# Performance work log

Measured on AMD Instinct MI355X. Metric: run time of the kernel, lower is better.

Reference implementation:

```python
import jax, jax.numpy as jnp
import numpy as np

N_NODES = 100000
N_EDGES = 200000
Z_DIM = 64
ATTR_DIM = 768
HID = 128
N_CLASSES = 5


def setup_inputs() -> dict:
    key = jax.random.key(0)
    ks = jax.random.split(key, 6)
    z = jax.random.normal(ks[0], (N_NODES, Z_DIM), dtype=jnp.float32)
    edge_index = jax.random.randint(ks[1], (2, N_EDGES), 0, N_NODES, dtype=jnp.int64)
    edge_attr = jax.random.normal(ks[2], (N_EDGES, ATTR_DIM), dtype=jnp.float32)
    W1 = jax.random.normal(ks[3], (ATTR_DIM + Z_DIM, HID), dtype=jnp.float32) * 0.02
    b1 = jnp.zeros((HID,), dtype=jnp.float32)
    W2 = jax.random.normal(ks[4], (HID, N_CLASSES), dtype=jnp.float32) * 0.02
    b2 = jnp.zeros((N_CLASSES,), dtype=jnp.float32)
    return {"z": z, "edge_index": edge_index, "edge_attr": edge_attr,
            "W1": W1, "b1": b1, "W2": W2, "b2": b2}


def reference(z, edge_index, edge_attr, W1, b1, W2, b2):
    # decode(): gather endpoint embeddings, elementwise product  [E, 64]
    node_rep = z[edge_index[0]] * z[edge_index[1]]
    # concat with edge attributes -> [E, 64 + 768] (torch cat order: node_rep first)
    joint = jnp.concatenate([node_rep, edge_attr], axis=-1)
    # 2-layer MLP + softmax
    h = jax.nn.relu(joint @ W1 + b1)
    logits = h @ W2 + b2
    return jax.nn.softmax(logits, axis=-1)
```

## Files before the change

### kernel.cpp

```cpp
#include <hip/hip_runtime.h>
#include <hip/hip_bf16.h>

#define E_TOT 200000
#define NZ 64
#define ATTR_D 768
#define HID_D 128
#define NCLS 5
#define NSTG 12

typedef __attribute__((ext_vector_type(8))) short short8;
typedef __attribute__((ext_vector_type(4))) float f32x4;

typedef __attribute__((address_space(3))) unsigned       lds_u32_t;
typedef const __attribute__((address_space(1))) unsigned glob_u32_t;

__device__ __forceinline__ unsigned pk2(float a, float b) {
    __hip_bfloat162 h = __float22bfloat162_rn(make_float2(a, b));
    return *reinterpret_cast<unsigned*>(&h);
}

__device__ __forceinline__ short8 pack8(const float4 x0, const float4 x1) {
    union { unsigned u[4]; short8 s; } r;
    r.u[0] = pk2(x0.x, x0.y);
    r.u[1] = pk2(x0.z, x0.w);
    r.u[2] = pk2(x1.x, x1.y);
    r.u[3] = pk2(x1.z, x1.w);
    return r.s;
}

__global__ void prep_w1f(const float* __restrict__ W1, __hip_bfloat16* __restrict__ w1f) {
    int idx = blockIdx.x * 256 + threadIdx.x;
    if (idx >= 26 * 8 * 64 * 8) return;
    int j    = idx & 7;
    int lane = (idx >> 3) & 63;
    int f    = (idx >> 9) & 7;
    int kt   = idx >> 12;
    int n = f * 16 + (lane & 15);
    int k = kt * 32 + (lane >> 4) * 8 + j;
    w1f[idx] = __float2bfloat16(W1[(size_t)k * HID_D + n]);
}

__global__ __launch_bounds__(256, 2) void gcn_main(
    const float* __restrict__ z, const int* __restrict__ ei,
    const float* __restrict__ attr, const __hip_bfloat16* __restrict__ w1f,
    const float* __restrict__ b1, const float* __restrict__ W2,
    const float* __restrict__ b2, float* __restrict__ out) {

    __shared__ float As[2][128 * 64];

    const int t    = threadIdx.x;
    const int wv   = t >> 6;
    const int lane = t & 63;
    const int g    = lane >> 4;
    const int c0   = lane & 15;
    const int e0   = blockIdx.x * 128;

    const float* sbase[8];
#pragma unroll
    for (int i = 0; i < 8; ++i) {
        int O   = wv * 1024 + i * 4096 + lane * 16;
        int row = O >> 8;
        int c   = (O >> 4) & 15;
        int er  = e0 + row; if (er >= E_TOT) er = E_TOT - 1;
        sbase[i] = attr + (size_t)er * ATTR_D + c * 4;
    }
    auto STAGE = [&](int buf, int s) {
#pragma unroll
        for (int i = 0; i < 8; ++i)
            __builtin_amdgcn_global_load_lds(
                (glob_u32_t*)(sbase[i] + s * 64),
                (lds_u32_t*)&As[buf][wv * 256 + i * 1024],
                16, 0, 0);
    };

    const __hip_bfloat16* wf = w1f + (size_t)lane * 8;
    auto LOADB = [&](int kt, short8(&b)[8]) {
#pragma unroll
        for (int f = 0; f < 8; ++f)
            b[f] = *reinterpret_cast<const short8*>(wf + (size_t)(kt * 8 + f) * 512);
    };

    f32x4 acc[2][8];
#pragma unroll
    for (int m = 0; m < 2; ++m)
#pragma unroll
        for (int f = 0; f < 8; ++f) acc[m][f] = (f32x4){0.f, 0.f, 0.f, 0.f};

    const float* zsp[2];
    const float* zdp[2];
#pragma unroll
    for (int m = 0; m < 2; ++m) {
        int e = e0 + wv * 32 + m * 16 + c0; if (e >= E_TOT) e = E_TOT - 1;
        zsp[m] = z + (size_t)ei[e] * NZ + g * 8;
        zdp[m] = z + (size_t)ei[E_TOT + e] * NZ + g * 8;
    }
    float4 zsr[2][2][2], zdr[2][2][2];
#pragma unroll
    for (int m = 0; m < 2; ++m)
#pragma unroll
        for (int kt = 0; kt < 2; ++kt)
#pragma unroll
            for (int h = 0; h < 2; ++h) {
                zsr[m][kt][h] = *reinterpret_cast<const float4*>(zsp[m] + kt * 32 + h * 4);
                zdr[m][kt][h] = *reinterpret_cast<const float4*>(zdp[m] + kt * 32 + h * 4);
            }
    short8 bz0[8], bz1[8];
    LOADB(0, bz0); LOADB(1, bz1);
    STAGE(0, 0);

#pragma unroll
    for (int kt = 0; kt < 2; ++kt) {
        short8 a[2];
#pragma unroll
        for (int m = 0; m < 2; ++m) {
            float4 x0, x1;
            x0.x = zsr[m][kt][0].x * zdr[m][kt][0].x;
            x0.y = zsr[m][kt][0].y * zdr[m][kt][0].y;
            x0.z = zsr[m][kt][0].z * zdr[m][kt][0].z;
            x0.w = zsr[m][kt][0].w * zdr[m][kt][0].w;
            x1.x = zsr[m][kt][1].x * zdr[m][kt][1].x;
            x1.y = zsr[m][kt][1].y * zdr[m][kt][1].y;
            x1.z = zsr[m][kt][1].z * zdr[m][kt][1].z;
            x1.w = zsr[m][kt][1].w * zdr[m][kt][1].w;
            a[m] = pack8(x0, x1);
        }
#pragma unroll
        for (int f = 0; f < 8; ++f) {
            short8 bb = kt ? bz1[f] : bz0[f];
            acc[0][f] = __builtin_amdgcn_mfma_f32_16x16x32_bf16(a[0], bb, acc[0][f], 0, 0, 0);
            acc[1][f] = __builtin_amdgcn_mfma_f32_16x16x32_bf16(a[1], bb, acc[1][f], 0, 0, 0);
        }
    }

    short8 bx0[8], bx1[8], by0[8], by1[8];
    LOADB(2, bx0); LOADB(3, bx1);
    STAGE(1, 1);

#define ITER(S, BC0, BC1, BN0, BN1)                                            \
    {                                                                          \
        asm volatile("s_waitcnt vmcnt(8)" ::: "memory");                       \
        __builtin_amdgcn_sched_barrier(0);                                     \
        __builtin_amdgcn_s_barrier();                                          \
        float4 x[2][2][2];                                                     \
        _Pragma("unroll")                                                      \
        for (int m = 0; m < 2; ++m) {                                          \
            int r = wv * 32 + m * 16 + c0;                                     \
            _Pragma("unroll")                                                  \
            for (int kk = 0; kk < 2; ++kk) {                                   \
                const float* p = &As[(S) & 1][r * 64 + kk * 32 + g * 8];       \
                x[m][kk][0] = *reinterpret_cast<const float4*>(p);             \
                x[m][kk][1] = *reinterpret_cast<const float4*>(p + 4);         \
            }                                                                  \
        }                                                                      \
        asm volatile("s_waitcnt lgkmcnt(0)" ::: "memory");                     \
        __builtin_amdgcn_sched_barrier(0);                                     \
        __builtin_amdgcn_s_barrier();                                          \
        if ((S) + 1 < NSTG) { LOADB(2 * (S) + 4, BN0); LOADB(2 * (S) + 5, BN1); } \
        if ((S) + 2 < NSTG) STAGE((S) & 1, (S) + 2);                           \
        __builtin_amdgcn_sched_barrier(0);                                     \
        _Pragma("unroll")                                                      \
        for (int kk = 0; kk < 2; ++kk) {                                       \
            short8 a0 = pack8(x[0][kk][0], x[0][kk][1]);                       \
            short8 a1 = pack8(x[1][kk][0], x[1][kk][1]);                       \
            _Pragma("unroll")                                                  \
            for (int f = 0; f < 8; ++f) {                                      \
                short8 bb = kk ? (BC1)[f] : (BC0)[f];                          \
                acc[0][f] = __builtin_amdgcn_mfma_f32_16x16x32_bf16(a0, bb, acc[0][f], 0, 0, 0); \
                acc[1][f] = __builtin_amdgcn_mfma_f32_16x16x32_bf16(a1, bb, acc[1][f], 0, 0, 0); \
            }                                                                  \
        }                                                                      \
    }

    ITER(0,  bx0, bx1, by0, by1)
    ITER(1,  by0, by1, bx0, bx1)
    ITER(2,  bx0, bx1, by0, by1)
    ITER(3,  by0, by1, bx0, bx1)
    ITER(4,  bx0, bx1, by0, by1)
    ITER(5,  by0, by1, bx0, bx1)
    ITER(6,  bx0, bx1, by0, by1)
    ITER(7,  by0, by1, bx0, bx1)
    ITER(8,  bx0, bx1, by0, by1)
    ITER(9,  by0, by1, bx0, bx1)
    ITER(10, bx0, bx1, by0, by1)
    ITER(11, by0, by1, bx0, bx1)
#undef ITER

    float b1v[8], w2v[8][NCLS];
#pragma unroll
    for (int f = 0; f < 8; ++f) {
        int col = f * 16 + c0;
        b1v[f] = b1[col];
#pragma unroll
        for (int cc = 0; cc < NCLS; ++cc) w2v[f][cc] = W2[col * NCLS + cc];
    }
    float b2v[NCLS];
#pragma unroll
    for (int cc = 0; cc < NCLS; ++cc) b2v[cc] = b2[cc];

#pragma unroll
    for (int m = 0; m < 2; ++m) {
#pragma unroll
        for (int i = 0; i < 4; ++i) {
            float lg[NCLS] = {0.f, 0.f, 0.f, 0.f, 0.f};
#pragma unroll
            for (int f = 0; f < 8; ++f) {
                float h = acc[m][f][i] + b1v[f];
                h = fmaxf(h, 0.f);
#pragma unroll
                for (int cc = 0; cc < NCLS; ++cc) lg[cc] = fmaf(h, w2v[f][cc], lg[cc]);
            }
#pragma unroll
            for (int mask = 1; mask < 16; mask <<= 1) {
#pragma unroll
                for (int cc = 0; cc < NCLS; ++cc) lg[cc] += __shfl_xor(lg[cc], mask);
            }
#pragma unroll
            for (int cc = 0; cc < NCLS; ++cc) lg[cc] += b2v[cc];

            float mx = fmaxf(fmaxf(fmaxf(lg[0], lg[1]), fmaxf(lg[2], lg[3])), lg[4]);
            float q[NCLS];
            float s = 0.f;
#pragma unroll
            for (int cc = 0; cc < NCLS; ++cc) { q[cc] = __expf(lg[cc] - mx); s += q[cc]; }
            float inv = 1.0f / s;
            float num = (c0 == 0) ? q[0] : (c0 == 1) ? q[1] : (c0 == 2) ? q[2]
                      : (c0 == 3) ? q[3] : q[4];
            int eo = e0 + wv * 32 + m * 16 + g * 4 + i;
            if (eo < E_TOT && c0 < NCLS) out[(size_t)eo * NCLS + c0] = num * inv;
        }
    }
}

extern "C" void kernel_launch(void* const* d_in, const int* in_sizes, int n_in,
                              void* d_out, int out_size, void* d_ws, size_t ws_size,
                              hipStream_t stream) {
    const float* z    = (const float*)d_in[0];
    const int*   ei   = (const int*)d_in[1];
    const float* attr = (const float*)d_in[2];
    const float* W1   = (const float*)d_in[3];
    const float* b1   = (const float*)d_in[4];
    const float* W2   = (const float*)d_in[5];
    const float* b2   = (const float*)d_in[6];
    float* out = (float*)d_out;
    __hip_bfloat16* w1f = (__hip_bfloat16*)d_ws;

    prep_w1f<<<(26 * 8 * 64 * 8 + 255) / 256, 256, 0, stream>>>(W1, w1f);
    const int nblk = (E_TOT + 127) / 128;
    gcn_main<<<nblk, 256, 0, stream>>>(z, ei, attr, w1f, b1, W2, b2, out);
}
```

Baseline: 195.9 us.

## Use per-wave 4-deep swizzled LDS pipeline without block barriers

Restructures the edge_attr staging so each wave loads only its own 32 rows into a private LDS slice, which removes the block-wide s_barrier calls. The pipeline moves from a double buffer of 64-column stages to a 4-deep ring of 32-column stages with vmcnt-based waits. An XOR swizzle on the column chunks is added to avoid LDS bank conflicts, and B-fragment loads become single-buffered per stage. This is meant to cut synchronisation stalls and keep more loads in flight, in exchange for more fine-grained iterations and tighter reliance on vmcnt ordering being correct.

```diff
diff --git a/kernel.cpp b/kernel.cpp
--- a/kernel.cpp
+++ b/kernel.cpp
@@ -6,7 +6,6 @@
 #define ATTR_D 768
 #define HID_D 128
 #define NCLS 5
-#define NSTG 12
 
 typedef __attribute__((ext_vector_type(8))) short short8;
 typedef __attribute__((ext_vector_type(4))) float f32x4;
@@ -46,7 +45,7 @@
     const float* __restrict__ b1, const float* __restrict__ W2,
     const float* __restrict__ b2, float* __restrict__ out) {
 
-    __shared__ float As[2][128 * 64];
+    __shared__ float As[4][4096];
 
     const int t    = threadIdx.x;
     const int wv   = t >> 6;
@@ -55,23 +54,26 @@
     const int c0   = lane & 15;
     const int e0   = blockIdx.x * 128;
 
-    const float* sbase[8];
-#pragma unroll
-    for (int i = 0; i < 8; ++i) {
-        int O   = wv * 1024 + i * 4096 + lane * 16;
-        int row = O >> 8;
-        int c   = (O >> 4) & 15;
-        int er  = e0 + row; if (er >= E_TOT) er = E_TOT - 1;
-        sbase[i] = attr + (size_t)er * ATTR_D + c * 4;
-    }
-    auto STAGE = [&](int buf, int s) {
-#pragma unroll
-        for (int i = 0; i < 8; ++i)
-            __builtin_amdgcn_global_load_lds(
-                (glob_u32_t*)(sbase[i] + s * 64),
-                (lds_u32_t*)&As[buf][wv * 256 + i * 1024],
-                16, 0, 0);
-    };
+    const float* sbase[4];
+#pragma unroll
+    for (int i = 0; i < 4; ++i) {
+        int rsl = i * 8 + (lane >> 3);
+        int cch = (lane & 7) ^ (rsl & 7);
+        int er  = e0 + wv * 32 + rsl; if (er >= E_TOT) er = E_TOT - 1;
+        sbase[i] = attr + (size_t)er * ATTR_D + cch * 4;
+    }
+
+#define SB __builtin_amdgcn_sched_barrier(0)
+#define WAITVM(N) asm volatile("s_waitcnt vmcnt(" #N ")" ::: "memory")
+#define STAGE(BUF, S)                                                          \
+    {                                                                          \
+        _Pragma("unroll")                                                      \
+        for (int i = 0; i < 4; ++i)                                            \
+            __builtin_amdgcn_global_load_lds(                                  \
+                (glob_u32_t*)(sbase[i] + (S) * 32),                            \
+                (lds_u32_t*)&As[BUF][wv * 1024 + i * 256],                     \
+                16, 0, 0);                                                     \
+    }
 
     const __hip_bfloat16* wf = w1f + (size_t)lane * 8;
     auto LOADB = [&](int kt, short8(&b)[8]) {
@@ -79,12 +81,6 @@
         for (int f = 0; f < 8; ++f)
             b[f] = *reinterpret_cast<const short8*>(wf + (size_t)(kt * 8 + f) * 512);
     };
-
-    f32x4 acc[2][8];
-#pragma unroll
-    for (int m = 0; m < 2; ++m)
-#pragma unroll
-        for (int f = 0; f < 8; ++f) acc[m][f] = (f32x4){0.f, 0.f, 0.f, 0.f};
 
     const float* zsp[2];
     const float* zdp[2];
@@ -104,9 +100,24 @@
                 zsr[m][kt][h] = *reinterpret_cast<const float4*>(zsp[m] + kt * 32 + h * 4);
                 zdr[m][kt][h] = *reinterpret_cast<const float4*>(zdp[m] + kt * 32 + h * 4);
             }
+    SB;
     short8 bz0[8], bz1[8];
     LOADB(0, bz0); LOADB(1, bz1);
-    STAGE(0, 0);
+    SB;
+    STAGE(0, 0); SB;
+    STAGE(1, 1); SB;
+    short8 bX[8], bY[8];
+    LOADB(2, bX);
+    SB;
+    STAGE(2, 2); SB;
+    LOADB(3, bY);
+    SB;
+
+    f32x4 acc[2][8];
+#pragma unroll
+    for (int m = 0; m < 2; ++m)
+#pragma unroll
+        for (int f = 0; f < 8; ++f) acc[m][f] = (f32x4){0.f, 0.f, 0.f, 0.f};
 
 #pragma unroll
     for (int kt = 0; kt < 2; ++kt) {
@@ -132,58 +143,57 @@
         }
     }
 
-    short8 bx0[8], bx1[8], by0[8], by1[8];
-    LOADB(2, bx0); LOADB(3, bx1);
-    STAGE(1, 1);
-
-#define ITER(S, BC0, BC1, BN0, BN1)                                            \
-    {                                                                          \
-        asm volatile("s_waitcnt vmcnt(8)" ::: "memory");                       \
-        __builtin_amdgcn_sched_barrier(0);                                     \
-        __builtin_amdgcn_s_barrier();                                          \
-        float4 x[2][2][2];                                                     \
+#define ITER_BODY(S, BC)                                                       \
+        const float* sl = &As[(S) & 3][wv * 1024];                             \
+        int pA = (2 * g) ^ (c0 & 7);                                           \
+        int pB = pA ^ 1;                                                       \
+        float4 x00 = *reinterpret_cast<const float4*>(sl + c0 * 32 + pA * 4);  \
+        float4 x01 = *reinterpret_cast<const float4*>(sl + c0 * 32 + pB * 4);  \
+        float4 x10 = *reinterpret_cast<const float4*>(sl + (c0 + 16) * 32 + pA * 4); \
+        float4 x11 = *reinterpret_cast<const float4*>(sl + (c0 + 16) * 32 + pB * 4); \
+        short8 a0 = pack8(x00, x01);                                           \
+        short8 a1 = pack8(x10, x11);                                           \
         _Pragma("unroll")                                                      \
-        for (int m = 0; m < 2; ++m) {                                          \
-            int r = wv * 32 + m * 16 + c0;                                     \
-            _Pragma("unroll")                                                  \
-            for (int kk = 0; kk < 2; ++kk) {                                   \
-                const float* p = &As[(S) & 1][r * 64 + kk * 32 + g * 8];       \
-                x[m][kk][0] = *reinterpret_cast<const float4*>(p);             \
-                x[m][kk][1] = *reinterpret_cast<const float4*>(p + 4);         \
-            }                                                                  \
-        }                                                                      \
-        asm volatile("s_waitcnt lgkmcnt(0)" ::: "memory");                     \
-        __builtin_amdgcn_sched_barrier(0);                                     \
-        __builtin_amdgcn_s_barrier();                                          \
-        if ((S) + 1 < NSTG) { LOADB(2 * (S) + 4, BN0); LOADB(2 * (S) + 5, BN1); } \
-        if ((S) + 2 < NSTG) STAGE((S) & 1, (S) + 2);                           \
-        __builtin_amdgcn_sched_barrier(0);                                     \
-        _Pragma("unroll")                                                      \
-        for (int kk = 0; kk < 2; ++kk) {                                       \
-            short8 a0 = pack8(x[0][kk][0], x[0][kk][1]);                       \
-            short8 a1 = pack8(x[1][kk][0], x[1][kk][1]);                       \
-            _Pragma("unroll")                                                  \
-            for (int f = 0; f < 8; ++f) {                                      \
-                short8 bb = kk ? (BC1)[f] : (BC0)[f];                          \
-                acc[0][f] = __builtin_amdgcn_mfma_f32_16x16x32_bf16(a0, bb, acc[0][f], 0, 0, 0); \
-                acc[1][f] = __builtin_amdgcn_mfma_f32_16x16x32_bf16(a1, bb, acc[1][f], 0, 0, 0); \
-            }                                                                  \
-        }                                                                      \
-    }
-
-    ITER(0,  bx0, bx1, by0, by1)
-    ITER(1,  by0, by1, bx0, bx1)
-    ITER(2,  bx0, bx1, by0, by1)
-    ITER(3,  by0, by1, bx0, bx1)
-    ITER(4,  bx0, bx1, by0, by1)
-    ITER(5,  by0, by1, bx0, bx1)
-    ITER(6,  bx0, bx1, by0, by1)
-    ITER(7,  by0, by1, bx0, bx1)
-    ITER(8,  bx0, bx1, by0, by1)
-    ITER(9,  by0, by1, bx0, bx1)
-    ITER(10, bx0, bx1, by0, by1)
-    ITER(11, by0, by1, bx0, bx1)
-#undef ITER
+        for (int f = 0; f < 8; ++f) {                                          \
+            acc[0][f] = __builtin_amdgcn_mfma_f32_16x16x32_bf16(a0, (BC)[f], acc[0][f], 0, 0, 0); \
+            acc[1][f] = __builtin_amdgcn_mfma_f32_16x16x32_bf16(a1, (BC)[f], acc[1][f], 0, 0, 0); \
+        }
+
+#define ITER_FULL(S, BC)                                                       \
+    {                                                                          \
+        WAITVM(12); SB;                                                        \
+        STAGE(((S) + 3) & 3, (S) + 3); SB;                                     \
+        ITER_BODY(S, BC)                                                       \
+        SB; LOADB((S) + 4, BC); SB;                                            \
+    }
+#define ITER_NOS(S, BC)                                                        \
+    {                                                                          \
+        WAITVM(12); SB;                                                        \
+        ITER_BODY(S, BC)                                                       \
+        SB; LOADB((S) + 4, BC); SB;                                            \
+    }
+#define ITER_BARE(S, W, BC)                                                    \
+    {                                                                          \
+        WAITVM(W); SB;                                                         \
+        ITER_BODY(S, BC)                                                       \
+    }
+
+    ITER_FULL(0,  bX) ITER_FULL(1,  bY) ITER_FULL(2,  bX) ITER_FULL(3,  bY)
+    ITER_FULL(4,  bX) ITER_FULL(5,  bY) ITER_FULL(6,  bX) ITER_FULL(7,  bY)
+    ITER_FULL(8,  bX) ITER_FULL(9,  bY) ITER_FULL(10, bX) ITER_FULL(11, bY)
+    ITER_FULL(12, bX) ITER_FULL(13, bY) ITER_FULL(14, bX) ITER_FULL(15, bY)
+    ITER_FULL(16, bX) ITER_FULL(17, bY) ITER_FULL(18, bX) ITER_FULL(19, bY)
+    ITER_FULL(20, bX)
+    ITER_NOS(21, bY)
+    ITER_BARE(22, 8, bX)
+    ITER_BARE(23, 0, bY)
+#undef ITER_FULL
+#undef ITER_NOS
+#undef ITER_BARE
+#undef ITER_BODY
+#undef STAGE
+#undef WAITVM
+#undef SB
 
     float b1v[8], w2v[8][NCLS];
 #pragma unroll
```

Measured after the change: 183.1 us. 6.5% less time.
